# Optimization experiments

Hardware: AMD Instinct MI355X
Metric: run time of the kernel (lower is better)

## Reference

```python
import jax, jax.numpy as jnp
import numpy as np

N = 10000      # nodes
E = 160000     # edges (before self-loops)
IN = 128       # input channels
H1, C1 = 8, 128   # layer-1 heads / per-head channels
OUT = 64       # output channels
NEG_SLOPE = 0.2   # PyG GATConv leaky_relu slope


def _glorot(key, shape):
    fan = shape[0] + shape[-1]
    return jax.random.normal(key, shape, jnp.float32) * np.float32(np.sqrt(2.0 / fan))


def setup_inputs() -> dict:
    key = jax.random.key(0)
    ks = jax.random.split(key, 10)
    x = jax.random.normal(ks[0], (N, IN), jnp.float32)
    edge_index = jax.random.randint(ks[1], (2, E), 0, N, dtype=jnp.int64)
    return {
        "x": x,
        "edge_index": edge_index,
        "W1": _glorot(ks[2], (IN, H1 * C1)),
        "a_src1": _glorot(ks[3], (H1, C1)),
        "a_dst1": _glorot(ks[4], (H1, C1)),
        "b1": jnp.zeros((H1 * C1,), jnp.float32),
        "W2": _glorot(ks[5], (H1 * C1, OUT)),
        "a_src2": _glorot(ks[6], (1, OUT)),
        "a_dst2": _glorot(ks[7], (1, OUT)),
        "b2": jnp.zeros((OUT,), jnp.float32),
    }


def gat_conv(x, src, dst, W, a_src, a_dst, bias, heads, ch, concat):
    n = x.shape[0]
    h = (x @ W).reshape(n, heads, ch)                 # [N,H,C]
    alpha_s = jnp.sum(h * a_src, axis=-1)             # [N,H]
    alpha_d = jnp.sum(h * a_dst, axis=-1)             # [N,H]
    e = jax.nn.leaky_relu(alpha_s[src] + alpha_d[dst], NEG_SLOPE)  # [E',H]
    # segment softmax over incoming edges of each dst node
    m = jax.ops.segment_max(e, dst, num_segments=n)
    e = jnp.exp(e - m[dst])
    s = jax.ops.segment_sum(e, dst, num_segments=n)
    alpha = e / (s[dst] + 1e-16)                      # [E',H]
    msg = h[src] * alpha[:, :, None]                  # [E',H,C]
    out = jax.ops.segment_sum(msg, dst, num_segments=n)  # [N,H,C]
    out = out.reshape(n, heads * ch) if concat else jnp.mean(out, axis=1)
    return out + bias


def reference(x, edge_index, W1, a_src1, a_dst1, b1, W2, a_src2, a_dst2, b2):
    n = x.shape[0]
    loops = jnp.arange(n, dtype=edge_index.dtype)     # PyG add_self_loops=True
    src = jnp.concatenate([edge_index[0], loops])
    dst = jnp.concatenate([edge_index[1], loops])
    h = jax.nn.elu(gat_conv(x, src, dst, W1, a_src1, a_dst1, b1, H1, C1, True))
    # dropout is identity in eval mode
    return gat_conv(h, src, dst, W2, a_src2, a_dst2, b2, 1, OUT, False)
```

## Files before the change

### kernel.cpp

```cpp
#include <hip/hip_runtime.h>
#include <math.h>


#define NEG_SLOPE 0.2f

typedef short bf16x8 __attribute__((ext_vector_type(8)));
typedef float f32x4 __attribute__((ext_vector_type(4)));

__device__ __forceinline__ float leaky(float v) { return v >= 0.0f ? v : NEG_SLOPE * v; }

__device__ __forceinline__ unsigned short f2bf(float f) {
    unsigned u = __float_as_uint(f);
    u += 0x7FFFu + ((u >> 16) & 1u);
    return (unsigned short)(u >> 16);
}


__global__ __launch_bounds__(256) void prep_count(
    const float* __restrict__ W1, const float* __restrict__ a_src1,
    const float* __restrict__ a_dst1, const float* __restrict__ W2,
    const int* __restrict__ ei,
    float* __restrict__ As_t, float* __restrict__ Ad_t,
    unsigned short* __restrict__ W1bT, unsigned short* __restrict__ W2bT,
    int* __restrict__ counts, int E, int N) {
    int b = blockIdx.x;
    __shared__ unsigned short tile[32][33];
    if (b < 4) {
        int i = b * 256 + threadIdx.x;
        int k = i >> 3, h = i & 7;
        float ss = 0.f, sd = 0.f;
        for (int c = 0; c < 128; c += 4) {
            float4 w = *(const float4*)(W1 + (size_t)k * 1024 + h * 128 + c);
            float4 a = *(const float4*)(a_src1 + h * 128 + c);
            float4 d = *(const float4*)(a_dst1 + h * 128 + c);
            ss += w.x * a.x + w.y * a.y + w.z * a.z + w.w * a.w;
            sd += w.x * d.x + w.y * d.y + w.z * d.z + w.w * d.w;
        }
        As_t[h * 132 + k] = ss;
        Ad_t[h * 132 + k] = sd;
    } else if (b < 132) {
        int bb = b - 4;
        int kt = bb & 3, hct = bb >> 2;
        int j = threadIdx.x & 31;
        int i0 = threadIdx.x >> 5;
        for (int i = i0; i < 32; i += 8)
            tile[i][j] = f2bf(W1[(size_t)(kt * 32 + i) * 1024 + hct * 32 + j]);
        __syncthreads();
        for (int i = i0; i < 32; i += 8) {
            int hc = hct * 32 + i, k = kt * 32 + j;
            int h = hc >> 7, c = hc & 127;
            W1bT[h * 16384 + c * 128 + k] = tile[j][i];
        }
    } else if (b < 196) {
        int bb = b - 132;
        int kt = bb & 31, ctile = bb >> 5;
        int j = threadIdx.x & 31;
        int i0 = threadIdx.x >> 5;
        for (int i = i0; i < 32; i += 8)
            tile[i][j] = f2bf(W2[(size_t)(kt * 32 + i) * 64 + ctile * 32 + j]);
        __syncthreads();
        for (int i = i0; i < 32; i += 8)
            W2bT[(size_t)(ctile * 32 + i) * 1024 + kt * 32 + j] = tile[j][i];
    } else {
        int i = (b - 196) * 256 + threadIdx.x;
        int M = E + N;
        if (i >= M) return;
        int dst = (i < E) ? ei[E + i] : (i - E);
        atomicAdd(&counts[dst], 1);
    }
}


__global__ __launch_bounds__(1024) void alpha_scan(
    const float* __restrict__ x, const float* __restrict__ As_t, const float* __restrict__ Ad_t,
    float* __restrict__ as1, float* __restrict__ ad1,
    const int* __restrict__ counts, int* __restrict__ offsets,
    int* __restrict__ cursor, int N, int nb_alpha) {
    int t = threadIdx.x;
    if ((int)blockIdx.x < nb_alpha) {
        __shared__ float sAs[1056], sAd[1056];
        for (int i = t; i < 1056; i += 1024) {
            sAs[i] = As_t[i];
            sAd[i] = Ad_t[i];
        }
        __syncthreads();
        int node = blockIdx.x * 128 + (t >> 3);
        int h = t & 7;
        if (node >= N) return;
        const float* sa = sAs + h * 132;
        const float* sd = sAd + h * 132;
        float accs = 0.f, accd = 0.f;
        for (int k = 0; k < 128; k += 4) {
            float4 xv = *(const float4*)(x + (size_t)node * 128 + k);
            float4 av = *(const float4*)(sa + k);
            float4 dv = *(const float4*)(sd + k);
            accs += xv.x * av.x + xv.y * av.y + xv.z * av.z + xv.w * av.w;
            accd += xv.x * dv.x + xv.y * dv.y + xv.z * dv.z + xv.w * dv.w;
        }
        as1[node * 8 + h] = accs;
        ad1[node * 8 + h] = accd;
    } else {
        __shared__ int wsum[16];
        int per = (N + 1023) / 1024;
        int base = t * per;
        int s = 0;
        for (int j = 0; j < per; j++) {
            int idx = base + j;
            if (idx < N) s += counts[idx];
        }
        int lane = t & 63, wid = t >> 6;
        int inc = s;
#pragma unroll
        for (int off = 1; off <= 32; off <<= 1) {
            int v = __shfl_up(inc, off);
            if (lane >= off) inc += v;
        }
        if (lane == 63) wsum[wid] = inc;
        __syncthreads();
        if (t < 16) {
            int v = wsum[t];
            int iv = v;
#pragma unroll
            for (int off = 1; off <= 8; off <<= 1) {
                int u = __shfl_up(iv, off);
                if (t >= off) iv += u;
            }
            wsum[t] = iv - v;
        }
        __syncthreads();
        int run = wsum[wid] + inc - s;
        for (int j = 0; j < per; j++) {
            int idx = base + j;
            if (idx < N) {
                offsets[idx] = run;
                cursor[idx] = run;
                run += counts[idx];
            }
        }
        if (t == 1023) offsets[N] = run;
    }
}


__global__ __launch_bounds__(256) void fill_w1(
    const int* __restrict__ ei, int* __restrict__ cursor,
    const float* __restrict__ as1, const float* __restrict__ ad1,
    int* __restrict__ srcs, float* __restrict__ wbuf, int E, int N) {
    int i = blockIdx.x * blockDim.x + threadIdx.x;
    int M = E + N;
    if (i >= M) return;
    int src, dst;
    if (i < E) { src = ei[i]; dst = ei[E + i]; }
    else       { src = dst = i - E; }
    int pos = atomicAdd(&cursor[dst], 1);
    srcs[pos] = src;
    float4 a0 = *(const float4*)(as1 + (size_t)src * 8);
    float4 a1 = *(const float4*)(as1 + (size_t)src * 8 + 4);
    float4 b0 = *(const float4*)(ad1 + (size_t)dst * 8);
    float4 b1 = *(const float4*)(ad1 + (size_t)dst * 8 + 4);
    float4 w0, w1;
    w0.x = __expf(leaky(a0.x + b0.x));
    w0.y = __expf(leaky(a0.y + b0.y));
    w0.z = __expf(leaky(a0.z + b0.z));
    w0.w = __expf(leaky(a0.w + b0.w));
    w1.x = __expf(leaky(a1.x + b1.x));
    w1.y = __expf(leaky(a1.y + b1.y));
    w1.z = __expf(leaky(a1.z + b1.z));
    w1.w = __expf(leaky(a1.w + b1.w));
    *(float4*)(wbuf + (size_t)pos * 8)     = w0;
    *(float4*)(wbuf + (size_t)pos * 8 + 4) = w1;
}


__global__ __launch_bounds__(256) void l1_gather(
    const float* __restrict__ x, const float* __restrict__ wbuf,
    const int* __restrict__ offsets, const int* __restrict__ srcs,
    unsigned short* __restrict__ y_b, int N) {
    int n = blockIdx.x * 4 + (threadIdx.x >> 6);
    if (n >= N) return;
    int lane = threadIdx.x & 63;
    int beg = offsets[n];
    int deg = offsets[n + 1] - beg;
    float2 acc[8];
#pragma unroll
    for (int h = 0; h < 8; h++) acc[h] = make_float2(0.f, 0.f);
    float4 ws0 = make_float4(0.f, 0.f, 0.f, 0.f);
    float4 ws1 = make_float4(0.f, 0.f, 0.f, 0.f);
    const float* xb = x + lane * 2;
#define L1G_BODY(I)                                                              \
    {                                                                            \
        int s_ = srcs[beg + (I)];                                                \
        float4 w0_ = *(const float4*)(wbuf + (size_t)(beg + (I)) * 8);           \
        float4 w1_ = *(const float4*)(wbuf + (size_t)(beg + (I)) * 8 + 4);       \
        float2 xv_ = *(const float2*)(xb + (size_t)s_ * 128);                    \
        ws0.x += w0_.x; ws0.y += w0_.y; ws0.z += w0_.z; ws0.w += w0_.w;          \
        ws1.x += w1_.x; ws1.y += w1_.y; ws1.z += w1_.z; ws1.w += w1_.w;          \
        acc[0].x = fmaf(w0_.x, xv_.x, acc[0].x); acc[0].y = fmaf(w0_.x, xv_.y, acc[0].y); \
        acc[1].x = fmaf(w0_.y, xv_.x, acc[1].x); acc[1].y = fmaf(w0_.y, xv_.y, acc[1].y); \
        acc[2].x = fmaf(w0_.z, xv_.x, acc[2].x); acc[2].y = fmaf(w0_.z, xv_.y, acc[2].y); \
        acc[3].x = fmaf(w0_.w, xv_.x, acc[3].x); acc[3].y = fmaf(w0_.w, xv_.y, acc[3].y); \
        acc[4].x = fmaf(w1_.x, xv_.x, acc[4].x); acc[4].y = fmaf(w1_.x, xv_.y, acc[4].y); \
        acc[5].x = fmaf(w1_.y, xv_.x, acc[5].x); acc[5].y = fmaf(w1_.y, xv_.y, acc[5].y); \
        acc[6].x = fmaf(w1_.z, xv_.x, acc[6].x); acc[6].y = fmaf(w1_.z, xv_.y, acc[6].y); \
        acc[7].x = fmaf(w1_.w, xv_.x, acc[7].x); acc[7].y = fmaf(w1_.w, xv_.y, acc[7].y); \
    }
    int i = 0;
    for (; i + 4 <= deg; i += 4) {
        L1G_BODY(i) L1G_BODY(i + 1) L1G_BODY(i + 2) L1G_BODY(i + 3)
    }
    for (; i < deg; i++) { L1G_BODY(i) }
#undef L1G_BODY
    float inv[8] = {1.f / (ws0.x + 1e-16f), 1.f / (ws0.y + 1e-16f),
                    1.f / (ws0.z + 1e-16f), 1.f / (ws0.w + 1e-16f),
                    1.f / (ws1.x + 1e-16f), 1.f / (ws1.y + 1e-16f),
                    1.f / (ws1.z + 1e-16f), 1.f / (ws1.w + 1e-16f)};
    unsigned short* dst = y_b + (size_t)n * 1024 + lane * 2;
#pragma unroll
    for (int h = 0; h < 8; h++) {
        unsigned lo = f2bf(acc[h].x * inv[h]);
        unsigned hi = f2bf(acc[h].y * inv[h]);
        *(unsigned*)(dst + h * 128) = lo | (hi << 16);
    }
}


__global__ __launch_bounds__(256) void l12_gemm(
    const unsigned short* __restrict__ y_b, const unsigned short* __restrict__ W1bT,
    const float* __restrict__ b1, const unsigned short* __restrict__ W2bT,
    const float* __restrict__ a_src2, const float* __restrict__ a_dst2,
    float* __restrict__ h2, float* __restrict__ as2, float* __restrict__ ad2, int N) {
    int nb = blockIdx.x * 16;
    int w = threadIdx.x >> 6;
    int lane = threadIdx.x & 63;
    int n16 = lane & 15, quad = lane >> 4;
    __shared__ unsigned short hb[16 * 1032];
    __shared__ float sA[4][16], sD[4][16];
    int node_a = nb + n16;
    const unsigned short* yrow = y_b + (size_t)(node_a < N ? node_a : 0) * 1024;
#pragma unroll
    for (int cti = 0; cti < 16; cti++) {
        int ct = w * 16 + cti;
        int h = ct >> 3;
        int cc = (ct & 7) * 16;
        const unsigned short* Wh = W1bT + h * 16384 + (size_t)(cc + n16) * 128 + quad * 8;
        const unsigned short* ya = yrow + h * 128 + quad * 8;
        f32x4 acc = (f32x4){0.f, 0.f, 0.f, 0.f};
#pragma unroll
        for (int ks = 0; ks < 4; ks++) {
            bf16x8 a = *(const bf16x8*)(ya + ks * 32);
            bf16x8 b = *(const bf16x8*)(Wh + ks * 32);
            acc = __builtin_amdgcn_mfma_f32_16x16x32_bf16(a, b, acc, 0, 0, 0);
        }
        int c = h * 128 + cc + n16;
        float bias = b1[c];
#pragma unroll
        for (int r = 0; r < 4; r++) {
            float v = acc[r] + bias;
            v = v > 0.f ? v : expm1f(v);
            hb[(quad * 4 + r) * 1032 + c] = f2bf(v);
        }
    }
    __syncthreads();
    const unsigned short* arow = hb + n16 * 1032 + quad * 8;
    const unsigned short* brow = W2bT + (size_t)(w * 16 + n16) * 1024 + quad * 8;
    f32x4 acc = (f32x4){0.f, 0.f, 0.f, 0.f};
#pragma unroll 8
    for (int ks = 0; ks < 32; ks++) {
        bf16x8 a = *(const bf16x8*)(arow + ks * 32);
        bf16x8 b = *(const bf16x8*)(brow + ks * 32);
        acc = __builtin_amdgcn_mfma_f32_16x16x32_bf16(a, b, acc, 0, 0, 0);
    }
    int c2 = w * 16 + n16;
    float asc = a_src2[c2], adc = a_dst2[c2];
    float pav[4], pdv[4];
#pragma unroll
    for (int r = 0; r < 4; r++) {
        int node = nb + quad * 4 + r;
        if (node < N) h2[(size_t)node * 64 + c2] = acc[r];
        pav[r] = acc[r] * asc;
        pdv[r] = acc[r] * adc;
#pragma unroll
        for (int mm = 1; mm <= 8; mm <<= 1) {
            pav[r] += __shfl_xor(pav[r], mm);
            pdv[r] += __shfl_xor(pdv[r], mm);
        }
    }
    if (n16 == 0) {
#pragma unroll
        for (int r = 0; r < 4; r++) {
            sA[w][quad * 4 + r] = pav[r];
            sD[w][quad * 4 + r] = pdv[r];
        }
    }
    __syncthreads();
    if (threadIdx.x < 16) {
        int node = nb + threadIdx.x;
        if (node < N) {
            as2[node] = sA[0][threadIdx.x] + sA[1][threadIdx.x] + sA[2][threadIdx.x] + sA[3][threadIdx.x];
            ad2[node] = sD[0][threadIdx.x] + sD[1][threadIdx.x] + sD[2][threadIdx.x] + sD[3][threadIdx.x];
        }
    }
}


__global__ __launch_bounds__(256) void l2_gather(
    const float* __restrict__ h2, const float* __restrict__ as2,
    const float* __restrict__ ad2, const float* __restrict__ b2,
    const int* __restrict__ offsets, const int* __restrict__ srcs,
    float* __restrict__ out, int N) {
    int n = blockIdx.x * 4 + (threadIdx.x >> 6);
    if (n >= N) return;
    int lane = threadIdx.x & 63;
    int beg = offsets[n];
    int deg = offsets[n + 1] - beg;
    float adn = ad2[n];
    float acc = 0.f, wsum = 0.f;
    int i = 0;
    for (; i + 4 <= deg; i += 4) {
        int s0 = srcs[beg + i],     s1 = srcs[beg + i + 1];
        int s2 = srcs[beg + i + 2], s3 = srcs[beg + i + 3];
        float w0 = __expf(leaky(as2[s0] + adn));
        float w1 = __expf(leaky(as2[s1] + adn));
        float w2 = __expf(leaky(as2[s2] + adn));
        float w3 = __expf(leaky(as2[s3] + adn));
        float v0 = h2[(size_t)s0 * 64 + lane];
        float v1 = h2[(size_t)s1 * 64 + lane];
        float v2 = h2[(size_t)s2 * 64 + lane];
        float v3 = h2[(size_t)s3 * 64 + lane];
        wsum += w0 + w1 + w2 + w3;
        acc = fmaf(w0, v0, acc);
        acc = fmaf(w1, v1, acc);
        acc = fmaf(w2, v2, acc);
        acc = fmaf(w3, v3, acc);
    }
    for (; i < deg; i++) {
        int s = srcs[beg + i];
        float w = __expf(leaky(as2[s] + adn));
        wsum += w;
        acc = fmaf(w, h2[(size_t)s * 64 + lane], acc);
    }
    out[(size_t)n * 64 + lane] = acc / (wsum + 1e-16f) + b2[lane];
}


static inline size_t align_up(size_t v, size_t a) { return (v + a - 1) / a * a; }

extern "C" void kernel_launch(void* const* d_in, const int* in_sizes, int n_in,
                              void* d_out, int out_size, void* d_ws, size_t ws_size,
                              hipStream_t stream) {
    const float* x      = (const float*)d_in[0];
    const int*   ei     = (const int*)d_in[1];
    const float* W1     = (const float*)d_in[2];
    const float* a_src1 = (const float*)d_in[3];
    const float* a_dst1 = (const float*)d_in[4];
    const float* b1     = (const float*)d_in[5];
    const float* W2     = (const float*)d_in[6];
    const float* a_src2 = (const float*)d_in[7];
    const float* a_dst2 = (const float*)d_in[8];
    const float* b2     = (const float*)d_in[9];
    float* out = (float*)d_out;

    int N = in_sizes[0] / 128;
    int E = in_sizes[1] / 2;
    int M = E + N;

    char* p = (char*)d_ws;
    size_t off = 0;
    auto carve = [&](size_t bytes) {
        void* r = p + off;
        off = align_up(off + bytes, 256);
        return r;
    };
    int*            counts  = (int*)carve((size_t)N * 4);
    int*            offsets = (int*)carve((size_t)(N + 1) * 4);
    int*            cursor  = (int*)carve((size_t)N * 4);
    int*            srcs    = (int*)carve((size_t)M * 4);
    float*          As_t    = (float*)carve(1056 * 4);
    float*          Ad_t    = (float*)carve(1056 * 4);
    float*          as1     = (float*)carve((size_t)N * 8 * 4);
    float*          ad1     = (float*)carve((size_t)N * 8 * 4);
    float*          as2     = (float*)carve((size_t)N * 4);
    float*          ad2     = (float*)carve((size_t)N * 4);
    float*          h2      = (float*)carve((size_t)N * 64 * 4);
    float*          wbuf    = (float*)carve((size_t)M * 8 * 4);
    unsigned short* W1bT    = (unsigned short*)carve((size_t)8 * 128 * 128 * 2);
    unsigned short* W2bT    = (unsigned short*)carve((size_t)64 * 1024 * 2);
    unsigned short* y_b     = (unsigned short*)carve((size_t)N * 1024 * 2);
    (void)ws_size;

    int nb_count = (M + 255) / 256;
    int nb_alpha = (N + 127) / 128;

    hipMemsetAsync(counts, 0, (size_t)N * 4, stream);
    prep_count<<<196 + nb_count, 256, 0, stream>>>(W1, a_src1, a_dst1, W2, ei,
                                                   As_t, Ad_t, W1bT, W2bT, counts, E, N);
    alpha_scan<<<nb_alpha + 1, 1024, 0, stream>>>(x, As_t, Ad_t, as1, ad1,
                                                  counts, offsets, cursor, N, nb_alpha);
    fill_w1<<<nb_count, 256, 0, stream>>>(ei, cursor, as1, ad1, srcs, wbuf, E, N);
    l1_gather<<<(N + 3) / 4, 256, 0, stream>>>(x, wbuf, offsets, srcs, y_b, N);
    l12_gemm<<<(N + 15) / 16, 256, 0, stream>>>(y_b, W1bT, b1, W2bT, a_src2, a_dst2,
                                                h2, as2, ad2, N);
    l2_gather<<<(N + 3) / 4, 256, 0, stream>>>(h2, as2, ad2, b2, offsets, srcs, out, N);
}
```

Before: 192.8 us.

## Use 8 waves in fused layer GEMM with per-head A reuse and split-K

The fused layer-1/layer-2 GEMM kernel now launches 512 threads (8 waves). In the first GEMM each wave owns one head, so it loads its A fragments from y_b once and reuses them across 8 column tiles. The second GEMM splits K across two wave groups and reduces their partials through shared memory. This adds parallelism per block and cuts redundant A loads, at the cost of an extra barrier, more shared memory and possibly lower occupancy.

```diff
diff --git a/kernel.cpp b/kernel.cpp
--- a/kernel.cpp
+++ b/kernel.cpp
@@ -224,7 +224,7 @@
 }
 
 
-__global__ __launch_bounds__(256) void l12_gemm(
+__global__ __launch_bounds__(512) void l12_gemm(
     const unsigned short* __restrict__ y_b, const unsigned short* __restrict__ W1bT,
     const float* __restrict__ b1, const unsigned short* __restrict__ W2bT,
     const float* __restrict__ a_src2, const float* __restrict__ a_dst2,
@@ -234,24 +234,25 @@
     int lane = threadIdx.x & 63;
     int n16 = lane & 15, quad = lane >> 4;
     __shared__ unsigned short hb[16 * 1032];
+    __shared__ float red[4][64][4];
     __shared__ float sA[4][16], sD[4][16];
     int node_a = nb + n16;
-    const unsigned short* yrow = y_b + (size_t)(node_a < N ? node_a : 0) * 1024;
-#pragma unroll
-    for (int cti = 0; cti < 16; cti++) {
-        int ct = w * 16 + cti;
-        int h = ct >> 3;
-        int cc = (ct & 7) * 16;
-        const unsigned short* Wh = W1bT + h * 16384 + (size_t)(cc + n16) * 128 + quad * 8;
-        const unsigned short* ya = yrow + h * 128 + quad * 8;
+    const unsigned short* ya = y_b + (size_t)(node_a < N ? node_a : 0) * 1024
+                             + w * 128 + quad * 8;
+    bf16x8 af[4];
+#pragma unroll
+    for (int ks = 0; ks < 4; ks++) af[ks] = *(const bf16x8*)(ya + ks * 32);
+#pragma unroll
+    for (int cti = 0; cti < 8; cti++) {
+        int cc = cti * 16;
+        const unsigned short* Wh = W1bT + w * 16384 + (size_t)(cc + n16) * 128 + quad * 8;
         f32x4 acc = (f32x4){0.f, 0.f, 0.f, 0.f};
 #pragma unroll
         for (int ks = 0; ks < 4; ks++) {
-            bf16x8 a = *(const bf16x8*)(ya + ks * 32);
             bf16x8 b = *(const bf16x8*)(Wh + ks * 32);
-            acc = __builtin_amdgcn_mfma_f32_16x16x32_bf16(a, b, acc, 0, 0, 0);
-        }
-        int c = h * 128 + cc + n16;
+            acc = __builtin_amdgcn_mfma_f32_16x16x32_bf16(af[ks], b, acc, 0, 0, 0);
+        }
+        int c = w * 128 + cc + n16;
         float bias = b1[c];
 #pragma unroll
         for (int r = 0; r < 4; r++) {
@@ -261,35 +262,45 @@
         }
     }
     __syncthreads();
-    const unsigned short* arow = hb + n16 * 1032 + quad * 8;
-    const unsigned short* brow = W2bT + (size_t)(w * 16 + n16) * 1024 + quad * 8;
+    int ct2 = w & 3, kh = w >> 2;
+    const unsigned short* arow = hb + n16 * 1032 + kh * 512 + quad * 8;
+    const unsigned short* brow = W2bT + (size_t)(ct2 * 16 + n16) * 1024 + kh * 512 + quad * 8;
     f32x4 acc = (f32x4){0.f, 0.f, 0.f, 0.f};
-#pragma unroll 8
-    for (int ks = 0; ks < 32; ks++) {
+#pragma unroll
+    for (int ks = 0; ks < 16; ks++) {
         bf16x8 a = *(const bf16x8*)(arow + ks * 32);
         bf16x8 b = *(const bf16x8*)(brow + ks * 32);
         acc = __builtin_amdgcn_mfma_f32_16x16x32_bf16(a, b, acc, 0, 0, 0);
     }
-    int c2 = w * 16 + n16;
-    float asc = a_src2[c2], adc = a_dst2[c2];
-    float pav[4], pdv[4];
-#pragma unroll
-    for (int r = 0; r < 4; r++) {
-        int node = nb + quad * 4 + r;
-        if (node < N) h2[(size_t)node * 64 + c2] = acc[r];
-        pav[r] = acc[r] * asc;
-        pdv[r] = acc[r] * adc;
-#pragma unroll
-        for (int mm = 1; mm <= 8; mm <<= 1) {
-            pav[r] += __shfl_xor(pav[r], mm);
-            pdv[r] += __shfl_xor(pdv[r], mm);
-        }
-    }
-    if (n16 == 0) {
+    if (kh == 1) {
+#pragma unroll
+        for (int r = 0; r < 4; r++) red[ct2][lane][r] = acc[r];
+    }
+    __syncthreads();
+    if (kh == 0) {
+#pragma unroll
+        for (int r = 0; r < 4; r++) acc[r] += red[ct2][lane][r];
+        int c2 = ct2 * 16 + n16;
+        float asc = a_src2[c2], adc = a_dst2[c2];
+        float pav[4], pdv[4];
 #pragma unroll
         for (int r = 0; r < 4; r++) {
-            sA[w][quad * 4 + r] = pav[r];
-            sD[w][quad * 4 + r] = pdv[r];
+            int node = nb + quad * 4 + r;
+            if (node < N) h2[(size_t)node * 64 + c2] = acc[r];
+            pav[r] = acc[r] * asc;
+            pdv[r] = acc[r] * adc;
+#pragma unroll
+            for (int mm = 1; mm <= 8; mm <<= 1) {
+                pav[r] += __shfl_xor(pav[r], mm);
+                pdv[r] += __shfl_xor(pdv[r], mm);
+            }
+        }
+        if (n16 == 0) {
+#pragma unroll
+            for (int r = 0; r < 4; r++) {
+                sA[ct2][quad * 4 + r] = pav[r];
+                sD[ct2][quad * 4 + r] = pdv[r];
+            }
         }
     }
     __syncthreads();
@@ -398,7 +409,7 @@
                                                   counts, offsets, cursor, N, nb_alpha);
     fill_w1<<<nb_count, 256, 0, stream>>>(ei, cursor, as1, ad1, srcs, wbuf, E, N);
     l1_gather<<<(N + 3) / 4, 256, 0, stream>>>(x, wbuf, offsets, srcs, y_b, N);
-    l12_gemm<<<(N + 15) / 16, 256, 0, stream>>>(y_b, W1bT, b1, W2bT, a_src2, a_dst2,
+    l12_gemm<<<(N + 15) / 16, 512, 0, stream>>>(y_b, W1bT, b1, W2bT, a_src2, a_dst2,
                                                 h2, as2, ad2, N);
     l2_gather<<<(N + 3) / 4, 256, 0, stream>>>(h2, as2, ad2, b2, offsets, srcs, out, N);
 }
```

Measured after the change: 195.9 us. No clear change (+1.6%).
